# Kernel optimization log

Hardware: AMD Instinct MI355X
Metric: run time of the kernel (lower is better)

The kernel has to match this reference:

```python
import jax, jax.numpy as jnp
import numpy as np

# bitsandbytes NF4 codebook (16 quantile values in [-1, 1])
NF4 = jnp.array([
    -1.0, -0.6961928009986877, -0.5250730514526367, -0.39491748809814453,
    -0.28444138169288635, -0.18477343022823334, -0.09105003625154495, 0.0,
    0.07958029955625534, 0.16093020141124725, 0.24611230194568634,
    0.33791524171829224, 0.44070982933044434, 0.5626170039176941,
    0.7229568362236328, 1.0], dtype=jnp.float32)
BLOCK = 64  # bnb default quantization blocksize


def dequant_nf4(codes, absmax):
    """codes: int array of 4-bit indices, absmax: per-64-elem-block scale."""
    flat = NF4[codes.reshape(-1)]                      # codebook lookup
    flat = flat.reshape(-1, BLOCK) * absmax[:, None]   # per-block rescale
    return flat.reshape(codes.shape)


def setup_inputs() -> dict:
    key = jax.random.key(0)
    k1, k2, k3, k4, k5 = jax.random.split(key, 5)
    B, S, IN, OUT, R = 4, 2048, 4096, 4096, 8
    x = jax.random.normal(k1, (B, S, IN), dtype=jnp.float32)
    codes_A = jax.random.randint(k2, (R, IN), 0, 16, dtype=jnp.int32)
    absmax_A = jax.random.uniform(k3, (R * IN // BLOCK,), dtype=jnp.float32)
    codes_B = jax.random.randint(k4, (OUT, R), 0, 16, dtype=jnp.int32)
    absmax_B = jax.random.uniform(k5, (OUT * R // BLOCK,), dtype=jnp.float32)
    return {"x": x, "codes_A": codes_A, "absmax_A": absmax_A,
            "codes_B": codes_B, "absmax_B": absmax_B}


def reference(x, codes_A, absmax_A, codes_B, absmax_B):
    SCALING = 32.0 / 8.0  # alpha / rank
    W_A = dequant_nf4(codes_A, absmax_A)   # [rank, in]
    W_B = dequant_nf4(codes_B, absmax_B)   # [out, rank]
    interm = jnp.einsum('bsi,ri->bsr', x, W_A)          # lora_A: x @ W_A^T
    out = jnp.einsum('bsr,or->bso', interm, W_B)        # lora_B
    return out * SCALING
```

## Files before the change

### kernel.cpp

```cpp
#include <hip/hip_runtime.h>


static __device__ __constant__ float NF4_TBL[16] = {
    -1.0f, -0.6961928009986877f, -0.5250730514526367f, -0.39491748809814453f,
    -0.28444138169288635f, -0.18477343022823334f, -0.09105003625154495f, 0.0f,
    0.07958029955625534f, 0.16093020141124725f, 0.24611230194568634f,
    0.33791524171829224f, 0.44070982933044434f, 0.5626170039176941f,
    0.7229568362236328f, 1.0f};

__global__ void nf4_dequant_kernel(const int* __restrict__ codesA,
                                   const float* __restrict__ absA,
                                   const int* __restrict__ codesB,
                                   const float* __restrict__ absB,
                                   float* __restrict__ wA,
                                   float* __restrict__ wBt,
                                   int n) {
    int id = blockIdx.x * blockDim.x + threadIdx.x;
    if (id < n) {
        wA[id] = NF4_TBL[codesA[id] & 15] * absA[id >> 6];
        const int o = id >> 3;
        const int r = id & 7;
        wBt[r * 4096 + o] = NF4_TBL[codesB[id] & 15] * absB[id >> 6];
    }
}

__global__ __launch_bounds__(256, 4) void lora_a_kernel(
    const float* __restrict__ x,
    const float* __restrict__ wA,
    float* __restrict__ interm) {
    constexpr int IN4 = 4096 / 4;

    const int t    = threadIdx.x;
    const int wave = t >> 6;
    const int lane = t & 63;
    const int r0   = blockIdx.x * 8 + 2 * wave;

    const float4* __restrict__ x0  = (const float4*)(x + (size_t)r0 * 4096);
    const float4* __restrict__ x1  = (const float4*)(x + (size_t)(r0 + 1) * 4096);
    const float4* __restrict__ wA4 = (const float4*)wA;

    float acc0[8], acc1[8];
    #pragma unroll
    for (int r = 0; r < 8; ++r) { acc0[r] = 0.f; acc1[r] = 0.f; }

    #pragma unroll 4
    for (int c = 0; c < 16; ++c) {
        const int idx = lane + 64 * c;
        const float4 xa = x0[idx];
        const float4 xb = x1[idx];
        #pragma unroll
        for (int r = 0; r < 8; ++r) {
            const float4 w = wA4[r * IN4 + idx];
            acc0[r] += xa.x * w.x + xa.y * w.y + xa.z * w.z + xa.w * w.w;
            acc1[r] += xb.x * w.x + xb.y * w.y + xb.z * w.z + xb.w * w.w;
        }
    }

    #pragma unroll
    for (int r = 0; r < 8; ++r) {
        float v0 = acc0[r], v1 = acc1[r];
        #pragma unroll
        for (int off = 32; off > 0; off >>= 1) {
            v0 += __shfl_down(v0, off, 64);
            v1 += __shfl_down(v1, off, 64);
        }
        if (lane == 0) {
            interm[(size_t)r0 * 8 + r]       = v0 * 4.0f;
            interm[(size_t)(r0 + 1) * 8 + r] = v1 * 4.0f;
        }
    }
}

__global__ __launch_bounds__(256, 8) void lora_b_kernel(
    const float* __restrict__ interm,
    const float* __restrict__ wBt,
    float* __restrict__ out) {
    const int t    = threadIdx.x;
    const int row0 = blockIdx.x * 4;

    float im[4][8];
    const float* __restrict__ ip = interm + (size_t)row0 * 8;
    #pragma unroll
    for (int m = 0; m < 4; ++m)
        #pragma unroll
        for (int r = 0; r < 8; ++r)
            im[m][r] = ip[m * 8 + r];

    const float4* __restrict__ wt = (const float4*)wBt;

    #pragma unroll
    for (int k = 0; k < 4; ++k) {
        const int og = t + 256 * k;
        float4 w[8];
        #pragma unroll
        for (int r = 0; r < 8; ++r) w[r] = wt[r * 1024 + og];

        #pragma unroll
        for (int m = 0; m < 4; ++m) {
            float4 s;
            s.x = im[m][0] * w[0].x + im[m][1] * w[1].x + im[m][2] * w[2].x
                + im[m][3] * w[3].x + im[m][4] * w[4].x + im[m][5] * w[5].x
                + im[m][6] * w[6].x + im[m][7] * w[7].x;
            s.y = im[m][0] * w[0].y + im[m][1] * w[1].y + im[m][2] * w[2].y
                + im[m][3] * w[3].y + im[m][4] * w[4].y + im[m][5] * w[5].y
                + im[m][6] * w[6].y + im[m][7] * w[7].y;
            s.z = im[m][0] * w[0].z + im[m][1] * w[1].z + im[m][2] * w[2].z
                + im[m][3] * w[3].z + im[m][4] * w[4].z + im[m][5] * w[5].z
                + im[m][6] * w[6].z + im[m][7] * w[7].z;
            s.w = im[m][0] * w[0].w + im[m][1] * w[1].w + im[m][2] * w[2].w
                + im[m][3] * w[3].w + im[m][4] * w[4].w + im[m][5] * w[5].w
                + im[m][6] * w[6].w + im[m][7] * w[7].w;
            ((float4*)(out + (size_t)(row0 + m) * 4096))[og] = s;
        }
    }
}

extern "C" void kernel_launch(void* const* d_in, const int* in_sizes, int n_in,
                              void* d_out, int out_size, void* d_ws, size_t ws_size,
                              hipStream_t stream) {
    const float* x        = (const float*)d_in[0];
    const int*   codes_A  = (const int*)d_in[1];
    const float* absmax_A = (const float*)d_in[2];
    const int*   codes_B  = (const int*)d_in[3];
    const float* absmax_B = (const float*)d_in[4];
    float* out = (float*)d_out;

    constexpr int NW = 8 * 4096;
    float* wA     = (float*)d_ws;
    float* wBt    = (float*)d_ws + NW;
    float* interm = (float*)d_ws + 2 * NW;

    nf4_dequant_kernel<<<(NW + 255) / 256, 256, 0, stream>>>(
        codes_A, absmax_A, codes_B, absmax_B, wA, wBt, NW);

    lora_a_kernel<<<8192 / 8, 256, 0, stream>>>(x, wA, interm);
    lora_b_kernel<<<8192 / 4, 256, 0, stream>>>(interm, wBt, out);
}
```

Before: 257.6 us.

## Fuse LoRA A and B projections into one kernel via shared memory

Merges the lora_A reduction kernel and the lora_B expansion kernel into a single kernel. Each block computes the rank-8 intermediate for 8 rows, stages it in shared memory, syncs, and then writes the 4096-wide outputs. This removes one kernel launch and the global round trip for the intermediate. In exchange, each block runs a read-heavy phase followed by a write-heavy phase with a barrier between them, and the B phase now uses 8 rows per block instead of 4.

Measured after the change: 298.6 us. 1.16x slower.

```diff
diff --git a/kernel.cpp b/kernel.cpp
--- a/kernel.cpp
+++ b/kernel.cpp
@@ -24,70 +24,61 @@
     }
 }
 
-__global__ __launch_bounds__(256, 4) void lora_a_kernel(
+__global__ __launch_bounds__(256, 4) void qlora_fused_kernel(
     const float* __restrict__ x,
     const float* __restrict__ wA,
-    float* __restrict__ interm) {
-    constexpr int IN4 = 4096 / 4;
+    const float* __restrict__ wBt,
+    float* __restrict__ out) {
+    constexpr int IN4  = 4096 / 4;
+    constexpr int ROWS = 8;
+
+    __shared__ float4 interm4[ROWS][2];
 
     const int t    = threadIdx.x;
     const int wave = t >> 6;
     const int lane = t & 63;
-    const int r0   = blockIdx.x * 8 + 2 * wave;
+    const int row0 = blockIdx.x * ROWS;
 
-    const float4* __restrict__ x0  = (const float4*)(x + (size_t)r0 * 4096);
-    const float4* __restrict__ x1  = (const float4*)(x + (size_t)(r0 + 1) * 4096);
-    const float4* __restrict__ wA4 = (const float4*)wA;
+    {
+        const int r0 = row0 + 2 * wave;
+        const float4* __restrict__ x0  = (const float4*)(x + (size_t)r0 * 4096);
+        const float4* __restrict__ x1  = (const float4*)(x + (size_t)(r0 + 1) * 4096);
+        const float4* __restrict__ wA4 = (const float4*)wA;
 
-    float acc0[8], acc1[8];
-    #pragma unroll
-    for (int r = 0; r < 8; ++r) { acc0[r] = 0.f; acc1[r] = 0.f; }
+        float acc0[8], acc1[8];
+        #pragma unroll
+        for (int r = 0; r < 8; ++r) { acc0[r] = 0.f; acc1[r] = 0.f; }
 
-    #pragma unroll 4
-    for (int c = 0; c < 16; ++c) {
-        const int idx = lane + 64 * c;
-        const float4 xa = x0[idx];
-        const float4 xb = x1[idx];
+        #pragma unroll 4
+        for (int c = 0; c < 16; ++c) {
+            const int idx = lane + 64 * c;
+            const float4 xa = x0[idx];
+            const float4 xb = x1[idx];
+            #pragma unroll
+            for (int r = 0; r < 8; ++r) {
+                const float4 w = wA4[r * IN4 + idx];
+                acc0[r] += xa.x * w.x + xa.y * w.y + xa.z * w.z + xa.w * w.w;
+                acc1[r] += xb.x * w.x + xb.y * w.y + xb.z * w.z + xb.w * w.w;
+            }
+        }
+
         #pragma unroll
         for (int r = 0; r < 8; ++r) {
-            const float4 w = wA4[r * IN4 + idx];
-            acc0[r] += xa.x * w.x + xa.y * w.y + xa.z * w.z + xa.w * w.w;
-            acc1[r] += xb.x * w.x + xb.y * w.y + xb.z * w.z + xb.w * w.w;
+            float v0 = acc0[r], v1 = acc1[r];
+            #pragma unroll
+            for (int off = 32; off > 0; off >>= 1) {
+                v0 += __shfl_down(v0, off, 64);
+                v1 += __shfl_down(v1, off, 64);
+            }
+            if (lane == 0) {
+                ((float*)interm4)[(2 * wave + 0) * 8 + r] = v0 * 4.0f;
+                ((float*)interm4)[(2 * wave + 1) * 8 + r] = v1 * 4.0f;
+            }
         }
     }
-
-    #pragma unroll
-    for (int r = 0; r < 8; ++r) {
-        float v0 = acc0[r], v1 = acc1[r];
-        #pragma unroll
-        for (int off = 32; off > 0; off >>= 1) {
-            v0 += __shfl_down(v0, off, 64);
-            v1 += __shfl_down(v1, off, 64);
-        }
-        if (lane == 0) {
-            interm[(size_t)r0 * 8 + r]       = v0 * 4.0f;
-            interm[(size_t)(r0 + 1) * 8 + r] = v1 * 4.0f;
-        }
-    }
-}
-
-__global__ __launch_bounds__(256, 8) void lora_b_kernel(
-    const float* __restrict__ interm,
-    const float* __restrict__ wBt,
-    float* __restrict__ out) {
-    const int t    = threadIdx.x;
-    const int row0 = blockIdx.x * 4;
-
-    float im[4][8];
-    const float* __restrict__ ip = interm + (size_t)row0 * 8;
-    #pragma unroll
-    for (int m = 0; m < 4; ++m)
-        #pragma unroll
-        for (int r = 0; r < 8; ++r)
-            im[m][r] = ip[m * 8 + r];
+    __syncthreads();
 
     const float4* __restrict__ wt = (const float4*)wBt;
-
     #pragma unroll
     for (int k = 0; k < 4; ++k) {
         const int og = t + 256 * k;
@@ -96,20 +87,18 @@
         for (int r = 0; r < 8; ++r) w[r] = wt[r * 1024 + og];
 
         #pragma unroll
-        for (int m = 0; m < 4; ++m) {
+        for (int m = 0; m < ROWS; ++m) {
+            const float4 i0 = interm4[m][0];
+            const float4 i1 = interm4[m][1];
             float4 s;
-            s.x = im[m][0] * w[0].x + im[m][1] * w[1].x + im[m][2] * w[2].x
-                + im[m][3] * w[3].x + im[m][4] * w[4].x + im[m][5] * w[5].x
-                + im[m][6] * w[6].x + im[m][7] * w[7].x;
-            s.y = im[m][0] * w[0].y + im[m][1] * w[1].y + im[m][2] * w[2].y
-                + im[m][3] * w[3].y + im[m][4] * w[4].y + im[m][5] * w[5].y
-                + im[m][6] * w[6].y + im[m][7] * w[7].y;
-            s.z = im[m][0] * w[0].z + im[m][1] * w[1].z + im[m][2] * w[2].z
-                + im[m][3] * w[3].z + im[m][4] * w[4].z + im[m][5] * w[5].z
-                + im[m][6] * w[6].z + im[m][7] * w[7].z;
-            s.w = im[m][0] * w[0].w + im[m][1] * w[1].w + im[m][2] * w[2].w
-                + im[m][3] * w[3].w + im[m][4] * w[4].w + im[m][5] * w[5].w
-                + im[m][6] * w[6].w + im[m][7] * w[7].w;
+            s.x = i0.x * w[0].x + i0.y * w[1].x + i0.z * w[2].x + i0.w * w[3].x
+                + i1.x * w[4].x + i1.y * w[5].x + i1.z * w[6].x + i1.w * w[7].x;
+            s.y = i0.x * w[0].y + i0.y * w[1].y + i0.z * w[2].y + i0.w * w[3].y
+                + i1.x * w[4].y + i1.y * w[5].y + i1.z * w[6].y + i1.w * w[7].y;
+            s.z = i0.x * w[0].z + i0.y * w[1].z + i0.z * w[2].z + i0.w * w[3].z
+                + i1.x * w[4].z + i1.y * w[5].z + i1.z * w[6].z + i1.w * w[7].z;
+            s.w = i0.x * w[0].w + i0.y * w[1].w + i0.z * w[2].w + i0.w * w[3].w
+                + i1.x * w[4].w + i1.y * w[5].w + i1.z * w[6].w + i1.w * w[7].w;
             ((float4*)(out + (size_t)(row0 + m) * 4096))[og] = s;
         }
     }
@@ -126,13 +115,11 @@
     float* out = (float*)d_out;
 
     constexpr int NW = 8 * 4096;
-    float* wA     = (float*)d_ws;
-    float* wBt    = (float*)d_ws + NW;
-    float* interm = (float*)d_ws + 2 * NW;
+    float* wA  = (float*)d_ws;
+    float* wBt = (float*)d_ws + NW;
 
     nf4_dequant_kernel<<<(NW + 255) / 256, 256, 0, stream>>>(
         codes_A, absmax_A, codes_B, absmax_B, wA, wBt, NW);
 
-    lora_a_kernel<<<8192 / 8, 256, 0, stream>>>(x, wA, interm);
-    lora_b_kernel<<<8192 / 4, 256, 0, stream>>>(interm, wBt, out);
+    qlora_fused_kernel<<<8192 / 8, 256, 0, stream>>>(x, wA, wBt, out);
 }
```
